# Kernel tuning notes

Measured on AMD Instinct MI355X. Metric: run time of the kernel, lower is better.

Reference implementation:

```python
import math
import jax, jax.numpy as jnp
import numpy as np

DIM = 128
NUM_PROJ = 256
B, H, SEQ = 2, 16, 4096


def _make_orthogonal_S(key):
    # Mirrors QJLWithOrthogonal.__init__: raw Gaussian, QR-orthogonalize each
    # dim-row chunk, scale by sqrt(dim).
    raw = jax.random.normal(key, (NUM_PROJ, DIM), dtype=jnp.float32)
    blocks = []
    for start in range(0, NUM_PROJ, DIM):
        block = raw[start:min(start + DIM, NUM_PROJ)]
        if block.shape[0] <= block.shape[1]:
            q, _ = jnp.linalg.qr(block.T)  # reduced QR of [dim, rows]
            blocks.append(q.T * np.float32(math.sqrt(DIM)))
        else:
            blocks.append(block)
    return jnp.concatenate(blocks, axis=0)[:NUM_PROJ]


def setup_inputs() -> dict:
    key = jax.random.key(0)
    kq, kk, ks = jax.random.split(key, 3)
    query = jax.random.normal(kq, (B, H, SEQ, DIM), dtype=jnp.float32)
    key_t = jax.random.normal(kk, (B, H, SEQ, DIM), dtype=jnp.float32)
    S = _make_orthogonal_S(ks)
    return {"query": query, "key": key_t, "S": S}


def reference(query, key, S):
    # quantize(key): sign of JL projection -> {-1, +1}, shape [B,H,S,m]
    z = jnp.sign(jnp.einsum('bhsd,md->bhsm', key, S))
    # estimate_inner_product(query, z): asymmetric estimator
    qp = jnp.einsum('bhsd,md->bhsm', query, S)
    scale = np.float32(math.sqrt(math.pi / 2) / NUM_PROJ)
    return scale * jnp.sum(qp * z, axis=-1)  # [B,H,S]
```

## Files before the change

### kernel.cpp

```cpp
#include <hip/hip_runtime.h>
#include <hip/hip_bf16.h>


#define DIM        128
#define NPROJ      256
#define TILE_T     32
#define NWG        4096
#define LDS_STRIDE 136
#define TAU        6.0e-3f
#define SCALE      0.0048957583489668f

typedef __attribute__((ext_vector_type(8))) short short8;
typedef __attribute__((ext_vector_type(4))) float f32x4;

static __device__ __forceinline__ unsigned short bf16_rne(float x){
    unsigned int u = __builtin_bit_cast(unsigned int, x);
    u += 0x7FFFu + ((u >> 16) & 1u);
    return (unsigned short)(u >> 16);
}

static __device__ __attribute__((noinline))
float ref_sign(const float* __restrict__ Kg, const float* __restrict__ S,
               int tok, int m){
    const float4* kr = (const float4*)(Kg + (size_t)tok * DIM);
    const float4* sr = (const float4*)(S  + (size_t)m   * DIM);
    float acc = 0.f;
#pragma unroll 4
    for (int d = 0; d < DIM/4; ++d){
        float4 k4 = kr[d];
        float4 s4 = sr[d];
        acc = __builtin_fmaf(k4.x, s4.x, acc);
        acc = __builtin_fmaf(k4.y, s4.y, acc);
        acc = __builtin_fmaf(k4.z, s4.z, acc);
        acc = __builtin_fmaf(k4.w, s4.w, acc);
    }
    return (acc > 0.f) ? 1.f : ((acc < 0.f) ? -1.f : 0.f);
}

__global__ void prep_s_kernel(const float* __restrict__ S,
                              unsigned short* __restrict__ shi,
                              unsigned short* __restrict__ slo){
    int t    = blockIdx.x * 256 + threadIdx.x;
    int lane = t & 63;
    int ms   = (t >> 6) & 3;
    int ks   = (t >> 8) & 3;
    int g    = (t >> 10) & 3;
    int m    = g*64 + ms*16 + (lane & 15);
    int d    = ks*32 + (lane >> 4)*8;
    const float4* p = (const float4*)(S + (size_t)m*DIM + d);
    float4 x0 = p[0], x1 = p[1];
    float xs[8] = {x0.x,x0.y,x0.z,x0.w, x1.x,x1.y,x1.z,x1.w};
    size_t base = ((size_t)t) * 8;
    unsigned long long h0=0,h1=0,l0=0,l1=0;
#pragma unroll
    for (int e = 0; e < 4; ++e){
        unsigned short hb = bf16_rne(xs[e]);
        float hf = __builtin_bit_cast(float, (unsigned int)hb << 16);
        h0 |= (unsigned long long)hb                    << (16*e);
        l0 |= (unsigned long long)bf16_rne(xs[e] - hf)  << (16*e);
    }
#pragma unroll
    for (int e = 0; e < 4; ++e){
        unsigned short hb = bf16_rne(xs[4+e]);
        float hf = __builtin_bit_cast(float, (unsigned int)hb << 16);
        h1 |= (unsigned long long)hb                      << (16*e);
        l1 |= (unsigned long long)bf16_rne(xs[4+e] - hf)  << (16*e);
    }
    *(unsigned long long*)(shi + base)     = h0;
    *(unsigned long long*)(shi + base + 4) = h1;
    *(unsigned long long*)(slo + base)     = l0;
    *(unsigned long long*)(slo + base + 4) = l1;
}

template<bool USE_TAB>
static __device__ __forceinline__
void load_afrags(const unsigned short* __restrict__ shi_tab,
                 const unsigned short* __restrict__ slo_tab,
                 const float* __restrict__ S,
                 int wave, int ks, int l16, int quad, int lane,
                 short8 ah[4], short8 al[4]){
    if (USE_TAB){
#pragma unroll
        for (int ms = 0; ms < 4; ++ms){
            size_t off = ((size_t)((wave*4 + ks)*4 + ms)*64 + lane)*8;
            ah[ms] = *(const short8*)(shi_tab + off);
            al[ms] = *(const short8*)(slo_tab + off);
        }
    } else {
#pragma unroll
        for (int ms = 0; ms < 4; ++ms){
            const float4* p = (const float4*)(S + (size_t)(wave*64 + ms*16 + l16)*DIM
                                              + ks*32 + quad*8);
            float4 x0 = p[0], x1 = p[1];
            float xs[8] = {x0.x,x0.y,x0.z,x0.w, x1.x,x1.y,x1.z,x1.w};
            short8 h, l;
#pragma unroll
            for (int e = 0; e < 8; ++e){
                unsigned short hb = bf16_rne(xs[e]);
                float hf = __builtin_bit_cast(float, (unsigned int)hb << 16);
                h[e] = (short)hb;
                l[e] = (short)bf16_rne(xs[e] - hf);
            }
            ah[ms] = h;
            al[ms] = l;
        }
    }
}

template<bool USE_TAB>
__global__ __launch_bounds__(256, 4)
void qjl_kernel(const float* __restrict__ Qg, const float* __restrict__ Kg,
                const float* __restrict__ S,
                const unsigned short* __restrict__ shi_tab,
                const unsigned short* __restrict__ slo_tab,
                float* __restrict__ out)
{
    __shared__ unsigned short khi[TILE_T * LDS_STRIDE];
    __shared__ unsigned short klo[TILE_T * LDS_STRIDE];
    __shared__ unsigned short qhi[TILE_T * LDS_STRIDE];
    __shared__ float red[4][TILE_T];

    const int tid  = threadIdx.x;
    const int wave = tid >> 6;
    const int lane = tid & 63;
    const int l16  = lane & 15;
    const int quad = lane >> 4;
    const int tok0 = blockIdx.x * TILE_T;

    {
        const float4* ksrc = (const float4*)(Kg + (size_t)tok0 * DIM);
        const float4* qsrc = (const float4*)(Qg + (size_t)tok0 * DIM);
        float4 kv[4], qv[4];
#pragma unroll
        for (int j = 0; j < 4; ++j){ kv[j] = ksrc[tid + j*256]; qv[j] = qsrc[tid + j*256]; }
#pragma unroll
        for (int j = 0; j < 4; ++j){
            int i   = tid + j*256;
            int row = i >> 5;
            int c   = i & 31;
            float kx[4] = {kv[j].x, kv[j].y, kv[j].z, kv[j].w};
            float qx[4] = {qv[j].x, qv[j].y, qv[j].z, qv[j].w};
            unsigned long long hp = 0, lp = 0, qp = 0;
#pragma unroll
            for (int e = 0; e < 4; ++e){
                unsigned short hb = bf16_rne(kx[e]);
                float hf = __builtin_bit_cast(float, (unsigned int)hb << 16);
                hp |= (unsigned long long)hb                   << (16*e);
                lp |= (unsigned long long)bf16_rne(kx[e] - hf) << (16*e);
                qp |= (unsigned long long)bf16_rne(qx[e])      << (16*e);
            }
            int base = row * LDS_STRIDE + c*4;
            *(unsigned long long*)(khi + base) = hp;
            *(unsigned long long*)(klo + base) = lp;
            *(unsigned long long*)(qhi + base) = qp;
        }
    }
    __syncthreads();

    f32x4 accC[4][2];
    f32x4 accQ[4][2];
#pragma unroll
    for (int ms = 0; ms < 4; ++ms)
#pragma unroll
        for (int ts = 0; ts < 2; ++ts){
            accC[ms][ts] = (f32x4){0.f,0.f,0.f,0.f};
            accQ[ms][ts] = (f32x4){0.f,0.f,0.f,0.f};
        }

#pragma unroll
    for (int ks = 0; ks < 4; ++ks){
        short8 ah[4], al[4];
        load_afrags<USE_TAB>(shi_tab, slo_tab, S, wave, ks, l16, quad, lane,
                             ah, al);
#pragma unroll
        for (int ts = 0; ts < 2; ++ts){
            const int off = (ts*16 + l16) * LDS_STRIDE + ks*32 + quad*8;
            short8 bk = *(const short8*)(khi + off);
            short8 bl = *(const short8*)(klo + off);
            short8 bq = *(const short8*)(qhi + off);
#pragma unroll
            for (int ms = 0; ms < 4; ++ms){
                accC[ms][ts] = __builtin_amdgcn_mfma_f32_16x16x32_bf16(ah[ms], bk, accC[ms][ts], 0,0,0);
                accC[ms][ts] = __builtin_amdgcn_mfma_f32_16x16x32_bf16(al[ms], bk, accC[ms][ts], 0,0,0);
                accC[ms][ts] = __builtin_amdgcn_mfma_f32_16x16x32_bf16(ah[ms], bl, accC[ms][ts], 0,0,0);
                accQ[ms][ts] = __builtin_amdgcn_mfma_f32_16x16x32_bf16(ah[ms], bq, accQ[ms][ts], 0,0,0);
            }
        }
    }

    float part0 = 0.f, part1 = 0.f;
#pragma unroll
    for (int ts = 0; ts < 2; ++ts){
#pragma unroll
        for (int ms = 0; ms < 4; ++ms){
#pragma unroll
            for (int r = 0; r < 4; ++r){
                float c = accC[ms][ts][r];
                float s = (c >= 0.f) ? 1.f : -1.f;
                if (__builtin_fabsf(c) < TAU)
                    s = ref_sign(Kg, S, tok0 + ts*16 + l16,
                                 wave*64 + ms*16 + quad*4 + r);
                float sv = s * accQ[ms][ts][r];
                if (ts) part1 += sv; else part0 += sv;
            }
        }
    }

    part0 += __shfl_xor(part0, 16, 64);
    part0 += __shfl_xor(part0, 32, 64);
    part1 += __shfl_xor(part1, 16, 64);
    part1 += __shfl_xor(part1, 32, 64);
    if (quad == 0){
        red[wave][l16]      = part0;
        red[wave][16 + l16] = part1;
    }
    __syncthreads();
    if (tid < TILE_T)
        out[tok0 + tid] = SCALE * (red[0][tid] + red[1][tid] + red[2][tid] + red[3][tid]);
}

extern "C" void kernel_launch(void* const* d_in, const int* in_sizes, int n_in,
                              void* d_out, int out_size, void* d_ws, size_t ws_size,
                              hipStream_t stream){
    const float* Qg = (const float*)d_in[0];
    const float* Kg = (const float*)d_in[1];
    const float* S  = (const float*)d_in[2];
    float* out = (float*)d_out;

    const size_t tab_elems = (size_t)NPROJ * DIM;
    const size_t need = 2 * tab_elems * sizeof(unsigned short);

    if (d_ws && ws_size >= need){
        unsigned short* shi = (unsigned short*)d_ws;
        unsigned short* slo = shi + tab_elems;
        prep_s_kernel<<<16, 256, 0, stream>>>(S, shi, slo);
        qjl_kernel<true><<<NWG, 256, 0, stream>>>(Qg, Kg, S, shi, slo, out);
    } else {
        qjl_kernel<false><<<NWG, 256, 0, stream>>>(Qg, Kg, S, nullptr, nullptr, out);
    }
}
```

Before: 184.4 us.

## Add persistent kernel caching S tables in LDS with register prefetch of tiles

Result: slower. 223.1 us (+21.0%).

```diff
diff --git a/kernel.cpp b/kernel.cpp
--- a/kernel.cpp
+++ b/kernel.cpp
@@ -6,9 +6,15 @@
 #define NPROJ      256
 #define TILE_T     32
 #define NWG        4096
+#define NBLK_P     256
+#define TILES_PB   (NWG / NBLK_P)
 #define LDS_STRIDE 136
 #define TAU        6.0e-3f
 #define SCALE      0.0048957583489668f
+
+#define SHI_ELEMS  32768
+#define TILE_ELEMS (TILE_T * LDS_STRIDE)
+#define SMEM_BYTES ((2*SHI_ELEMS + 3*TILE_ELEMS) * 2 + 4 * TILE_T * 4)
 
 typedef __attribute__((ext_vector_type(8))) short short8;
 typedef __attribute__((ext_vector_type(4))) float f32x4;
@@ -72,6 +78,154 @@
     *(unsigned long long*)(slo + base + 4) = l1;
 }
 
+
+__global__ __launch_bounds__(256, 1)
+void qjl_persistent(const float* __restrict__ Qg, const float* __restrict__ Kg,
+                    const float* __restrict__ S,
+                    const unsigned short* __restrict__ shi_tab,
+                    const unsigned short* __restrict__ slo_tab,
+                    float* __restrict__ out)
+{
+    extern __shared__ unsigned short smem_us[];
+    unsigned short* s_hi = smem_us;
+    unsigned short* s_lo = s_hi + SHI_ELEMS;
+    unsigned short* khi  = s_lo + SHI_ELEMS;
+    unsigned short* klo  = khi + TILE_ELEMS;
+    unsigned short* qhi  = klo + TILE_ELEMS;
+    float* red = (float*)(qhi + TILE_ELEMS);
+
+    const int tid  = threadIdx.x;
+    const int wave = tid >> 6;
+    const int lane = tid & 63;
+    const int l16  = lane & 15;
+    const int quad = lane >> 4;
+
+    {
+        const short8* gh = (const short8*)shi_tab;
+        const short8* gl = (const short8*)slo_tab;
+        short8* lh = (short8*)s_hi;
+        short8* ll = (short8*)s_lo;
+#pragma unroll
+        for (int j = 0; j < 16; ++j){
+            int c = tid + j*256;
+            lh[c] = gh[c];
+            ll[c] = gl[c];
+        }
+    }
+
+    float4 kv[4], qv[4];
+    {
+        const size_t t0 = (size_t)blockIdx.x * TILES_PB * TILE_T * DIM;
+        const float4* ksrc = (const float4*)(Kg + t0);
+        const float4* qsrc = (const float4*)(Qg + t0);
+#pragma unroll
+        for (int j = 0; j < 4; ++j){ kv[j] = ksrc[tid + j*256]; qv[j] = qsrc[tid + j*256]; }
+    }
+
+#pragma unroll 1
+    for (int it = 0; it < TILES_PB; ++it){
+        const int tok0 = (blockIdx.x * TILES_PB + it) * TILE_T;
+
+#pragma unroll
+        for (int j = 0; j < 4; ++j){
+            int i   = tid + j*256;
+            int row = i >> 5;
+            int c   = i & 31;
+            float kx[4] = {kv[j].x, kv[j].y, kv[j].z, kv[j].w};
+            float qx[4] = {qv[j].x, qv[j].y, qv[j].z, qv[j].w};
+            unsigned long long hp = 0, lp = 0, qp = 0;
+#pragma unroll
+            for (int e = 0; e < 4; ++e){
+                unsigned short hb = bf16_rne(kx[e]);
+                float hf = __builtin_bit_cast(float, (unsigned int)hb << 16);
+                hp |= (unsigned long long)hb                   << (16*e);
+                lp |= (unsigned long long)bf16_rne(kx[e] - hf) << (16*e);
+                qp |= (unsigned long long)bf16_rne(qx[e])      << (16*e);
+            }
+            int base = row * LDS_STRIDE + c*4;
+            *(unsigned long long*)(khi + base) = hp;
+            *(unsigned long long*)(klo + base) = lp;
+            *(unsigned long long*)(qhi + base) = qp;
+        }
+        __syncthreads();
+
+        if (it + 1 < TILES_PB){
+            const size_t tn = (size_t)(tok0 + TILE_T) * DIM;
+            const float4* ksrc = (const float4*)(Kg + tn);
+            const float4* qsrc = (const float4*)(Qg + tn);
+#pragma unroll
+            for (int j = 0; j < 4; ++j){ kv[j] = ksrc[tid + j*256]; qv[j] = qsrc[tid + j*256]; }
+        }
+
+        f32x4 accC[4][2];
+        f32x4 accQ[4][2];
+#pragma unroll
+        for (int ms = 0; ms < 4; ++ms)
+#pragma unroll
+            for (int ts = 0; ts < 2; ++ts){
+                accC[ms][ts] = (f32x4){0.f,0.f,0.f,0.f};
+                accQ[ms][ts] = (f32x4){0.f,0.f,0.f,0.f};
+            }
+
+#pragma unroll
+        for (int ks = 0; ks < 4; ++ks){
+            short8 ah[4], al[4];
+#pragma unroll
+            for (int ms = 0; ms < 4; ++ms){
+                int off = (((wave*4 + ks)*4 + ms)*64 + lane)*8;
+                ah[ms] = *(const short8*)(s_hi + off);
+                al[ms] = *(const short8*)(s_lo + off);
+            }
+#pragma unroll
+            for (int ts = 0; ts < 2; ++ts){
+                const int off = (ts*16 + l16) * LDS_STRIDE + ks*32 + quad*8;
+                short8 bk = *(const short8*)(khi + off);
+                short8 bl = *(const short8*)(klo + off);
+                short8 bq = *(const short8*)(qhi + off);
+#pragma unroll
+                for (int ms = 0; ms < 4; ++ms){
+                    accC[ms][ts] = __builtin_amdgcn_mfma_f32_16x16x32_bf16(ah[ms], bk, accC[ms][ts], 0,0,0);
+                    accC[ms][ts] = __builtin_amdgcn_mfma_f32_16x16x32_bf16(al[ms], bk, accC[ms][ts], 0,0,0);
+                    accC[ms][ts] = __builtin_amdgcn_mfma_f32_16x16x32_bf16(ah[ms], bl, accC[ms][ts], 0,0,0);
+                    accQ[ms][ts] = __builtin_amdgcn_mfma_f32_16x16x32_bf16(ah[ms], bq, accQ[ms][ts], 0,0,0);
+                }
+            }
+        }
+
+        float part0 = 0.f, part1 = 0.f;
+#pragma unroll
+        for (int ts = 0; ts < 2; ++ts){
+#pragma unroll
+            for (int ms = 0; ms < 4; ++ms){
+#pragma unroll
+                for (int r = 0; r < 4; ++r){
+                    float c = accC[ms][ts][r];
+                    float s = (c >= 0.f) ? 1.f : -1.f;
+                    if (__builtin_fabsf(c) < TAU)
+                        s = ref_sign(Kg, S, tok0 + ts*16 + l16,
+                                     wave*64 + ms*16 + quad*4 + r);
+                    float sv = s * accQ[ms][ts][r];
+                    if (ts) part1 += sv; else part0 += sv;
+                }
+            }
+        }
+
+        part0 += __shfl_xor(part0, 16, 64);
+        part0 += __shfl_xor(part0, 32, 64);
+        part1 += __shfl_xor(part1, 16, 64);
+        part1 += __shfl_xor(part1, 32, 64);
+        if (quad == 0){
+            red[wave*TILE_T + l16]      = part0;
+            red[wave*TILE_T + 16 + l16] = part1;
+        }
+        __syncthreads();
+        if (tid < TILE_T)
+            out[tok0 + tid] = SCALE * (red[0*TILE_T + tid] + red[1*TILE_T + tid] +
+                                       red[2*TILE_T + tid] + red[3*TILE_T + tid]);
+    }
+}
+
+
 template<bool USE_TAB>
 static __device__ __forceinline__
 void load_afrags(const unsigned short* __restrict__ shi_tab,
@@ -170,8 +324,7 @@
 #pragma unroll
     for (int ks = 0; ks < 4; ++ks){
         short8 ah[4], al[4];
-        load_afrags<USE_TAB>(shi_tab, slo_tab, S, wave, ks, l16, quad, lane,
-                             ah, al);
+        load_afrags<USE_TAB>(shi_tab, slo_tab, S, wave, ks, l16, quad, lane, ah, al);
 #pragma unroll
         for (int ts = 0; ts < 2; ++ts){
             const int off = (ts*16 + l16) * LDS_STRIDE + ks*32 + quad*8;
@@ -230,11 +383,23 @@
     const size_t tab_elems = (size_t)NPROJ * DIM;
     const size_t need = 2 * tab_elems * sizeof(unsigned short);
 
+    static int attr_ok = -1;
+    if (attr_ok < 0){
+        hipError_t e = hipFuncSetAttribute(
+            reinterpret_cast<const void*>(&qjl_persistent),
+            hipFuncAttributeMaxDynamicSharedMemorySize, SMEM_BYTES);
+        attr_ok = (e == hipSuccess) ? 1 : 0;
+    }
+
     if (d_ws && ws_size >= need){
         unsigned short* shi = (unsigned short*)d_ws;
         unsigned short* slo = shi + tab_elems;
         prep_s_kernel<<<16, 256, 0, stream>>>(S, shi, slo);
-        qjl_kernel<true><<<NWG, 256, 0, stream>>>(Qg, Kg, S, shi, slo, out);
+        if (attr_ok){
+            qjl_persistent<<<NBLK_P, 256, SMEM_BYTES, stream>>>(Qg, Kg, S, shi, slo, out);
+        } else {
+            qjl_kernel<true><<<NWG, 256, 0, stream>>>(Qg, Kg, S, shi, slo, out);
+        }
     } else {
         qjl_kernel<false><<<NWG, 256, 0, stream>>>(Qg, Kg, S, nullptr, nullptr, out);
     }
```
